# Optimization experiments

Measured on AMD Instinct MI355X. Metric: run time of the kernel, lower is better.

Reference implementation:

```python
import jax, jax.numpy as jnp
import numpy as np

F, V, D, B = 3, 512, 8192, 64


def setup_inputs() -> dict:
    key = jax.random.key(0)
    k1, k2 = jax.random.split(key)
    # bipolar (MAP) codebooks: (f, v, d) in {-1, +1}
    codebooks = jnp.sign(jax.random.normal(k1, (F, V, D), dtype=jnp.float32))
    codebooks = jnp.where(codebooks == 0, 1.0, codebooks)
    # ground-truth factors -> inputs = bind (elementwise product) of one codevector per factor
    idx = jax.random.randint(k2, (B, F), 0, V)
    picked = codebooks[jnp.arange(F)[None, :], idx]          # (b, f, d)
    inputs = jnp.prod(picked, axis=1)                         # (b, d)
    # init estimates: bundle (superposition) of each codebook, signed, broadcast to batch
    init = jnp.sign(jnp.sum(codebooks, axis=1))               # (f, d)
    init = jnp.where(init == 0, 1.0, init)
    init_estimates = jnp.broadcast_to(init, (B, F, D)).astype(jnp.float32)
    return {"inputs": inputs, "init_estimates": init_estimates,
            "codebooks": codebooks, "iterations": 10}


def reference(inputs, init_estimates, codebooks, iterations):
    f = init_estimates.shape[-2]

    def step(est):
        # MAP inverse is identity; inv_others[:, j] = prod_{i != j} est[:, i]
        rolled = jnp.stack([jnp.roll(est, i, axis=-2) for i in range(1, f)], axis=-2)  # (b,f,f-1,d)
        inv_others = jnp.prod(rolled, axis=-2)                 # (b, f, d)  multibind
        new_est = inputs[:, None, :] * inv_others              # bind       (b, f, d)
        sim = jnp.einsum('bfd,fvd->bfv', new_est, codebooks)   # codebook similarity
        return jnp.sign(jnp.einsum('bfv,fvd->bfd', sim, codebooks))

    def cond(c):
        est, old, cnt, done = c
        return (cnt < iterations) & jnp.logical_not(done)

    def body(c):
        est, old, cnt, done = c
        new = step(est)
        done = jnp.all(new == old)
        return (new, new, cnt + 1, done)

    carry0 = (init_estimates, init_estimates, jnp.int32(0), jnp.array(False))
    est, _, cnt, _ = jax.lax.while_loop(cond, body, carry0)

    # cleanup: nearest codevector per factor (argmax dot similarity)
    sims = jnp.einsum('bfd,fvd->bfv', est, codebooks)
    outcome = jnp.argmax(sims, axis=-1)                        # (b, f) int indices
    return outcome, cnt - 1
```

## Files before the change

kernel.cpp:

```cpp
#include <hip/hip_runtime.h>

#define F 3
#define V 512
#define D 8192
#define B 64
#define ITERS 10
#define DW 256

typedef __bf16 bf16_t;
typedef __bf16 bf16x8 __attribute__((ext_vector_type(8)));
typedef float f32x4 __attribute__((ext_vector_type(4)));
typedef unsigned int u32;
typedef unsigned short u16;
typedef u16 u16x8 __attribute__((ext_vector_type(8)));
typedef unsigned long long u64;


__global__ __launch_bounds__(256) void k_init_tr(const float* __restrict__ Csrc,
                                                 u32* __restrict__ Cbits,
                                                 u32* __restrict__ CbTb,
                                                 int* __restrict__ flags) {
  int f = blockIdx.z, vt = blockIdx.y, dt = blockIdx.x;
  __shared__ bf16_t tile[64 * 65];
  int t = threadIdx.x;
  int lane = t & 63;
  int v0 = vt * 64, d0 = dt * 64;
  if (f == 0 && vt == 0 && dt == 0 && t < 32) flags[t] = 0;
#pragma unroll
  for (int p = 0; p < 16; ++p) {
    int q = t + 256 * p;
    int i = q >> 6, j = q & 63;
    float x = Csrc[((long)(f * V + v0 + i)) * D + d0 + j];
    tile[i * 65 + j] = (bf16_t)x;
    u64 bal = __ballot(x < 0.f);
    if (lane == 0) {
      int v = v0 + i;
      uint2 wp;
      wp.x = (u32)(bal & 0xffffffffull);
      wp.y = (u32)(bal >> 32);
      *(uint2*)&Cbits[(((f * 64 + (dt >> 1)) * 512) + v) * 4 + (dt & 1) * 2] = wp;
    }
  }
  __syncthreads();
#pragma unroll
  for (int p = 0; p < 16; ++p) {
    int q = t + 256 * p;
    int jj = q >> 6, ii = q & 63;
    float xv = (float)tile[ii * 65 + jj];
    u64 bal = __ballot(xv < 0.f);
    if (lane == 0) {
      int d = d0 + jj;
      uint2 wp;
      wp.x = (u32)(bal & 0xffffffffull);
      wp.y = (u32)(bal >> 32);
      *(uint2*)&CbTb[((long)f * D + d) * 16 + vt * 2] = wp;
    }
  }
}

__global__ void k_init_pack(const float* __restrict__ inputs, const float* __restrict__ ie,
                            u32* __restrict__ in_bits, u32* __restrict__ es0,
                            u32* __restrict__ ez0, int* __restrict__ flags) {
  int tid = blockIdx.x * blockDim.x + threadIdx.x;
  int lane = tid & 63;
  int gw = tid >> 6;
  int NW = (gridDim.x * blockDim.x) >> 6;
  const int IN_W = B * (D / 64);
  const int EST_W = B * F * (D / 64);
  for (int c = gw; c < IN_W + EST_W; c += NW) {
    if (c < IN_W) {
      int b = c >> 7, dc = c & 127;
      float x = inputs[(long)b * D + dc * 64 + lane];
      u64 bal = __ballot(x < 0.f);
      if (lane == 0) {
        in_bits[b * DW + dc * 2] = (u32)(bal & 0xffffffffull);
        in_bits[b * DW + dc * 2 + 1] = (u32)(bal >> 32);
      }
    } else {
      int cc = c - IN_W;
      int bf = cc >> 7, dc = cc & 127;
      float x = ie[(long)bf * D + dc * 64 + lane];
      u64 bs = __ballot(x < 0.f);
      u64 bz = __ballot(x == 0.f);
      if (lane == 0) {
        es0[bf * DW + dc * 2] = (u32)(bs & 0xffffffffull);
        es0[bf * DW + dc * 2 + 1] = (u32)(bs >> 32);
        ez0[bf * DW + dc * 2] = (u32)(bz & 0xffffffffull);
        ez0[bf * DW + dc * 2 + 1] = (u32)(bz >> 32);
        if (bz) atomicOr(&flags[16], 1);
      }
    }
  }
}

__global__ __launch_bounds__(512) void k_sim(const u32* __restrict__ Cbits,
                                             const u32* __restrict__ in_bits,
                                             const u32* __restrict__ es0,
                                             const u32* __restrict__ ez0,
                                             const u32* __restrict__ es1,
                                             const u32* __restrict__ ez1,
                                             int* __restrict__ sim,
                                             const int* __restrict__ flags, int iter) {
  const int t = threadIdx.x, lane = t & 63, w = t >> 6;
  const int gw = blockIdx.x * 8 + w;
  const int vg = gw & 7, b = (gw >> 3) & 63, fs = gw >> 9;
  const bool is_final = (iter >= ITERS);
  const u32 *es, *ez;
  if (is_final) {
    int first0 = ITERS;
    for (int i = 0; i < ITERS; ++i)
      if (flags[i] == 0) { first0 = i; break; }
    int par = (first0 < ITERS) ? ((first0 + 1) & 1) : 0;
    es = par ? es1 : es0;
    ez = par ? ez1 : ez0;
  } else {
    for (int i = 0; i < iter; ++i)
      if (flags[i] == 0) return;
    es = (iter & 1) ? es1 : es0;
    ez = (iter & 1) ? ez1 : ez0;
  }
  const int hz = flags[16];

  u32 As[4], Az[4];
  if (is_final) {
    const int i0 = (b * F + fs) * DW;
#pragma unroll
    for (int r = 0; r < 4; ++r) As[r] = es[i0 + r * 64 + lane];
    if (hz) {
#pragma unroll
      for (int r = 0; r < 4; ++r) Az[r] = ~ez[i0 + r * 64 + lane];
    }
  } else {
    const int f1 = (fs + 1) % 3, f2 = (fs + 2) % 3;
    const int a0 = (b * F + f1) * DW, a1 = (b * F + f2) * DW;
    const int n0 = b * DW;
#pragma unroll
    for (int r = 0; r < 4; ++r) {
      int o = r * 64 + lane;
      As[r] = in_bits[n0 + o] ^ es[a0 + o] ^ es[a1 + o];
    }
    if (hz) {
#pragma unroll
      for (int r = 0; r < 4; ++r) {
        int o = r * 64 + lane;
        Az[r] = ~(ez[a0 + o] | ez[a1 + o]);
      }
    }
  }

  int nzc = D;
  if (hz) {
    int p0 = 0;
#pragma unroll
    for (int r = 0; r < 4; ++r) p0 += __popc(Az[r]);
    for (int off = 32; off; off >>= 1) p0 += __shfl_xor(p0, off, 64);
    nzc = p0;
  }

  int acc = 0;
  const uint4* Cp = (const uint4*)Cbits + ((long)fs * 64) * 512 + vg * 64 + lane;
  if (!hz) {
#pragma unroll
    for (int r = 0; r < 4; ++r) {
#pragma unroll
      for (int i = 0; i < 16; ++i) {
        uint4 c = Cp[(r * 16 + i) * 512];
        const int k = i * 4;
        u32 a;
        a = (u32)__builtin_amdgcn_readlane((int)As[r], k + 0); acc += __popc(c.x ^ a);
        a = (u32)__builtin_amdgcn_readlane((int)As[r], k + 1); acc += __popc(c.y ^ a);
        a = (u32)__builtin_amdgcn_readlane((int)As[r], k + 2); acc += __popc(c.z ^ a);
        a = (u32)__builtin_amdgcn_readlane((int)As[r], k + 3); acc += __popc(c.w ^ a);
      }
    }
  } else {
#pragma unroll
    for (int r = 0; r < 4; ++r) {
#pragma unroll
      for (int i = 0; i < 16; ++i) {
        uint4 c = Cp[(r * 16 + i) * 512];
        const int k = i * 4;
        u32 a, z;
        a = (u32)__builtin_amdgcn_readlane((int)As[r], k + 0);
        z = (u32)__builtin_amdgcn_readlane((int)Az[r], k + 0); acc += __popc((c.x ^ a) & z);
        a = (u32)__builtin_amdgcn_readlane((int)As[r], k + 1);
        z = (u32)__builtin_amdgcn_readlane((int)Az[r], k + 1); acc += __popc((c.y ^ a) & z);
        a = (u32)__builtin_amdgcn_readlane((int)As[r], k + 2);
        z = (u32)__builtin_amdgcn_readlane((int)Az[r], k + 2); acc += __popc((c.z ^ a) & z);
        a = (u32)__builtin_amdgcn_readlane((int)As[r], k + 3);
        z = (u32)__builtin_amdgcn_readlane((int)Az[r], k + 3); acc += __popc((c.w ^ a) & z);
      }
    }
  }
  sim[(fs * B + b) * V + vg * 64 + lane] = nzc - 2 * acc;
}

__global__ __launch_bounds__(512) void k_upd(const int* __restrict__ sim,
                                             const u32* __restrict__ CbTb,
                                             u32* __restrict__ es0, u32* __restrict__ ez0,
                                             u32* __restrict__ es1, u32* __restrict__ ez1,
                                             int* __restrict__ flags, int iter) {
  const int fu = blockIdx.x >> 6;
  const int dt = blockIdx.x & 63, d0 = dt * 128;
  for (int i = 0; i < iter; ++i)
    if (flags[i] == 0) return;
  const u32* esIn = (iter & 1) ? es1 : es0;
  const u32* ezIn = (iter & 1) ? ez1 : ez0;
  u32* esOut = (iter & 1) ? es0 : es1;
  u32* ezOut = (iter & 1) ? ez0 : ez1;
  const int* simf = sim + fu * (B * V);

  __shared__ __attribute__((aligned(16))) bf16_t lAh[64 * 88];
  __shared__ __attribute__((aligned(16))) bf16_t lAl[64 * 88];
  __shared__ __attribute__((aligned(16))) bf16_t lB[128 * 88];

  const int t = threadIdx.x;
  const int lane = t & 63, w = t >> 6;
  const int lm = lane & 15, quad = lane >> 4;
  const int wd = w & 3, wm = w >> 2;

  f32x4 zero = {0.f, 0.f, 0.f, 0.f};
  f32x4 accH[2][2], accL[2][2];
#pragma unroll
  for (int m = 0; m < 2; ++m)
#pragma unroll
    for (int nt = 0; nt < 2; ++nt) { accH[m][nt] = zero; accL[m][nt] = zero; }

  for (int c = 0; c < 8; ++c) {
    const int vb = c * 64;
    __syncthreads();
    {
      int b8 = t >> 3, vv = (t & 7) * 8;
      const int* sp = simf + b8 * V + vb + vv;
      int4 sa = ((const int4*)sp)[0];
      int4 sb = ((const int4*)sp)[1];
      int si[8] = {sa.x, sa.y, sa.z, sa.w, sb.x, sb.y, sb.z, sb.w};
#pragma unroll
      for (int i = 0; i < 8; ++i) {
        lAh[b8 * 88 + vv + i] = (bf16_t)(float)(si[i] >> 8);
        lAl[b8 * 88 + vv + i] = (bf16_t)(float)(si[i] & 255);
      }
    }
#pragma unroll
    for (int p = 0; p < 2; ++p) {
      int q = t + 512 * p;
      int r = q >> 3, vv = (q & 7) * 8;
      u32 bits = CbTb[((long)fu * D + d0 + r) * 16 + ((vb + vv) >> 5)];
      int sh = (vb + vv) & 31;
      u16x8 o;
#pragma unroll
      for (int i = 0; i < 8; ++i)
        o[i] = (u16)(0x3F80u | (((bits >> (sh + i)) & 1u) << 15));
      *(u16x8*)&lB[r * 88 + vv] = o;
    }
    __syncthreads();
#pragma unroll
    for (int ks2 = 0; ks2 < 2; ++ks2) {
      const int kb = ks2 * 32 + quad * 8;
      bf16x8 bf0 = *(const bf16x8*)&lB[(wd * 32 + lm) * 88 + kb];
      bf16x8 bf1 = *(const bf16x8*)&lB[(wd * 32 + 16 + lm) * 88 + kb];
#pragma unroll
      for (int m = 0; m < 2; ++m) {
        const int mt = wm * 2 + m;
        bf16x8 ah = *(const bf16x8*)&lAh[(mt * 16 + lm) * 88 + kb];
        bf16x8 al = *(const bf16x8*)&lAl[(mt * 16 + lm) * 88 + kb];
        accH[m][0] = __builtin_amdgcn_mfma_f32_16x16x32_bf16(ah, bf0, accH[m][0], 0, 0, 0);
        accH[m][1] = __builtin_amdgcn_mfma_f32_16x16x32_bf16(ah, bf1, accH[m][1], 0, 0, 0);
        accL[m][0] = __builtin_amdgcn_mfma_f32_16x16x32_bf16(al, bf0, accL[m][0], 0, 0, 0);
        accL[m][1] = __builtin_amdgcn_mfma_f32_16x16x32_bf16(al, bf1, accL[m][1], 0, 0, 0);
      }
    }
  }
  const int W = dt * 4 + wd;
  bool anyd = false, zf = false;
#pragma unroll
  for (int m = 0; m < 2; ++m)
#pragma unroll
    for (int r = 0; r < 4; ++r) {
      float v0 = 256.f * accH[m][0][r] + accL[m][0][r];
      float v1 = 256.f * accH[m][1][r] + accL[m][1][r];
      u64 s0 = __ballot(v0 < 0.f);
      u64 s1 = __ballot(v1 < 0.f);
      u64 z0 = __ballot(v0 == 0.f);
      u64 z1 = __ballot(v1 == 0.f);
      zf |= ((z0 | z1) != 0ull);
      if (lm == 0) {
        u32 ws = (u32)((s0 >> (quad * 16)) & 0xffffull) |
                 (((u32)((s1 >> (quad * 16)) & 0xffffull)) << 16);
        u32 wz = (u32)((z0 >> (quad * 16)) & 0xffffull) |
                 (((u32)((z1 >> (quad * 16)) & 0xffffull)) << 16);
        int b = (wm * 2 + m) * 16 + quad * 4 + r;
        int idx = (b * F + fu) * DW + W;
        anyd |= (esIn[idx] != ws) || (ezIn[idx] != wz);
        esOut[idx] = ws;
        ezOut[idx] = wz;
      }
    }
  if (__any(anyd) && lane == 0) atomicOr(&flags[iter], 1);
  if (zf && lane == 0) atomicOr(&flags[16], 1);
}

__global__ __launch_bounds__(64) void k_out(const int* __restrict__ sim,
                                            const int* __restrict__ flags,
                                            int* __restrict__ out) {
  int bid = blockIdx.x;
  int b = bid / F, f = bid % F;
  int lane = threadIdx.x;
  const int* row = sim + (f * B + b) * V;
  int best = -2147483647;
  int bidx = 0;
#pragma unroll
  for (int i = 0; i < V / 64; ++i) {
    int v = lane + 64 * i;
    int x = row[v];
    if (x > best) { best = x; bidx = v; }
  }
  for (int off = 32; off; off >>= 1) {
    int ov = __shfl_down(best, off, 64);
    int oi = __shfl_down(bidx, off, 64);
    if (ov > best || (ov == best && oi < bidx)) { best = ov; bidx = oi; }
  }
  if (lane == 0) out[b * F + f] = bidx;
  if (bid == 0 && lane == 0) {
    int first0 = ITERS;
    for (int i = 0; i < ITERS; ++i) {
      if (flags[i] == 0) { first0 = i; break; }
    }
    int cnt = (first0 < ITERS) ? (first0 + 1) : ITERS;
    out[B * F] = cnt - 1;
  }
}

extern "C" void kernel_launch(void* const* d_in, const int* in_sizes, int n_in,
                              void* d_out, int out_size, void* d_ws, size_t ws_size,
                              hipStream_t stream) {
  const float* inputs    = (const float*)d_in[0];
  const float* init_est  = (const float*)d_in[1];
  const float* codebooks = (const float*)d_in[2];

  char* w = (char*)d_ws;
  size_t o = 0;
  auto alloc = [&](size_t bytes) -> void* {
    void* p = w + o;
    o = (o + bytes + 255) & ~(size_t)255;
    return p;
  };
  u32* Cbits   = (u32*)alloc((size_t)F * 64 * 512 * 4 * 4);
  u32* CbTb    = (u32*)alloc((size_t)F * D * 16 * 4);
  u32* in_bits = (u32*)alloc((size_t)B * DW * 4);
  u32* es0     = (u32*)alloc((size_t)B * F * DW * 4);
  u32* ez0     = (u32*)alloc((size_t)B * F * DW * 4);
  u32* es1     = (u32*)alloc((size_t)B * F * DW * 4);
  u32* ez1     = (u32*)alloc((size_t)B * F * DW * 4);
  int* sim     = (int*)alloc((size_t)F * B * V * 4);
  int* flags   = (int*)alloc(128);

  k_init_tr<<<dim3(128, 8, 3), 256, 0, stream>>>(codebooks, Cbits, CbTb, flags);
  k_init_pack<<<1024, 256, 0, stream>>>(inputs, init_est, in_bits, es0, ez0, flags);

  for (int j = 0; j < ITERS; ++j) {
    k_sim<<<192, 512, 0, stream>>>(Cbits, in_bits, es0, ez0, es1, ez1, sim, flags, j);
    k_upd<<<192, 512, 0, stream>>>(sim, CbTb, es0, ez0, es1, ez1, flags, j);
  }
  k_sim<<<192, 512, 0, stream>>>(Cbits, in_bits, es0, ez0, es1, ez1, sim, flags, ITERS);
  k_out<<<B * F, 64, 0, stream>>>(sim, flags, (int*)d_out);
}
```

Measured before the change: 533.9 us.

## Fuse iteration loop into one persistent kernel with software grid barriers

Replaces the 21 per-iteration launches of k_sim/k_upd plus k_out with a single persistent kernel of 192 blocks that alternates similarity and update phases, separated by an atomic counter/generation grid barrier. Convergence is checked in-kernel so all blocks break out together, and the argmax output step runs in the same kernel. This removes launch gaps and the early-exit flag scanning, in exchange for relying on all 192 blocks being co-resident and on the correctness of the hand-written barrier's fences.

```diff
diff --git a/kernel.cpp b/kernel.cpp
--- a/kernel.cpp
+++ b/kernel.cpp
@@ -6,6 +6,7 @@
 #define B 64
 #define ITERS 10
 #define DW 256
+#define NBLK 192
 
 typedef __bf16 bf16_t;
 typedef __bf16 bf16x8 __attribute__((ext_vector_type(8)));
@@ -15,6 +16,10 @@
 typedef u16 u16x8 __attribute__((ext_vector_type(8)));
 typedef unsigned long long u64;
 
+
+__device__ inline int aload(const int* p) {
+  return __hip_atomic_load((int*)p, __ATOMIC_RELAXED, __HIP_MEMORY_SCOPE_AGENT);
+}
 
 __global__ __launch_bounds__(256) void k_init_tr(const float* __restrict__ Csrc,
                                                  u32* __restrict__ Cbits,
@@ -25,7 +30,7 @@
   int t = threadIdx.x;
   int lane = t & 63;
   int v0 = vt * 64, d0 = dt * 64;
-  if (f == 0 && vt == 0 && dt == 0 && t < 32) flags[t] = 0;
+  if (f == 0 && vt == 0 && dt == 0 && t < 64) flags[t] = 0;
 #pragma unroll
   for (int p = 0; p < 16; ++p) {
     int q = t + 256 * p;
@@ -93,240 +98,248 @@
   }
 }
 
-__global__ __launch_bounds__(512) void k_sim(const u32* __restrict__ Cbits,
-                                             const u32* __restrict__ in_bits,
-                                             const u32* __restrict__ es0,
-                                             const u32* __restrict__ ez0,
-                                             const u32* __restrict__ es1,
-                                             const u32* __restrict__ ez1,
-                                             int* __restrict__ sim,
-                                             const int* __restrict__ flags, int iter) {
-  const int t = threadIdx.x, lane = t & 63, w = t >> 6;
-  const int gw = blockIdx.x * 8 + w;
-  const int vg = gw & 7, b = (gw >> 3) & 63, fs = gw >> 9;
-  const bool is_final = (iter >= ITERS);
-  const u32 *es, *ez;
-  if (is_final) {
-    int first0 = ITERS;
-    for (int i = 0; i < ITERS; ++i)
-      if (flags[i] == 0) { first0 = i; break; }
-    int par = (first0 < ITERS) ? ((first0 + 1) & 1) : 0;
-    es = par ? es1 : es0;
-    ez = par ? ez1 : ez0;
-  } else {
-    for (int i = 0; i < iter; ++i)
-      if (flags[i] == 0) return;
-    es = (iter & 1) ? es1 : es0;
-    ez = (iter & 1) ? ez1 : ez0;
-  }
-  const int hz = flags[16];
-
-  u32 As[4], Az[4];
-  if (is_final) {
-    const int i0 = (b * F + fs) * DW;
-#pragma unroll
-    for (int r = 0; r < 4; ++r) As[r] = es[i0 + r * 64 + lane];
-    if (hz) {
-#pragma unroll
-      for (int r = 0; r < 4; ++r) Az[r] = ~ez[i0 + r * 64 + lane];
-    }
-  } else {
-    const int f1 = (fs + 1) % 3, f2 = (fs + 2) % 3;
-    const int a0 = (b * F + f1) * DW, a1 = (b * F + f2) * DW;
-    const int n0 = b * DW;
-#pragma unroll
-    for (int r = 0; r < 4; ++r) {
-      int o = r * 64 + lane;
-      As[r] = in_bits[n0 + o] ^ es[a0 + o] ^ es[a1 + o];
-    }
-    if (hz) {
-#pragma unroll
-      for (int r = 0; r < 4; ++r) {
-        int o = r * 64 + lane;
-        Az[r] = ~(ez[a0 + o] | ez[a1 + o]);
-      }
-    }
-  }
-
-  int nzc = D;
-  if (hz) {
-    int p0 = 0;
-#pragma unroll
-    for (int r = 0; r < 4; ++r) p0 += __popc(Az[r]);
-    for (int off = 32; off; off >>= 1) p0 += __shfl_xor(p0, off, 64);
-    nzc = p0;
-  }
-
-  int acc = 0;
-  const uint4* Cp = (const uint4*)Cbits + ((long)fs * 64) * 512 + vg * 64 + lane;
-  if (!hz) {
-#pragma unroll
-    for (int r = 0; r < 4; ++r) {
-#pragma unroll
-      for (int i = 0; i < 16; ++i) {
-        uint4 c = Cp[(r * 16 + i) * 512];
-        const int k = i * 4;
-        u32 a;
-        a = (u32)__builtin_amdgcn_readlane((int)As[r], k + 0); acc += __popc(c.x ^ a);
-        a = (u32)__builtin_amdgcn_readlane((int)As[r], k + 1); acc += __popc(c.y ^ a);
-        a = (u32)__builtin_amdgcn_readlane((int)As[r], k + 2); acc += __popc(c.z ^ a);
-        a = (u32)__builtin_amdgcn_readlane((int)As[r], k + 3); acc += __popc(c.w ^ a);
-      }
-    }
-  } else {
-#pragma unroll
-    for (int r = 0; r < 4; ++r) {
-#pragma unroll
-      for (int i = 0; i < 16; ++i) {
-        uint4 c = Cp[(r * 16 + i) * 512];
-        const int k = i * 4;
-        u32 a, z;
-        a = (u32)__builtin_amdgcn_readlane((int)As[r], k + 0);
-        z = (u32)__builtin_amdgcn_readlane((int)Az[r], k + 0); acc += __popc((c.x ^ a) & z);
-        a = (u32)__builtin_amdgcn_readlane((int)As[r], k + 1);
-        z = (u32)__builtin_amdgcn_readlane((int)Az[r], k + 1); acc += __popc((c.y ^ a) & z);
-        a = (u32)__builtin_amdgcn_readlane((int)As[r], k + 2);
-        z = (u32)__builtin_amdgcn_readlane((int)Az[r], k + 2); acc += __popc((c.z ^ a) & z);
-        a = (u32)__builtin_amdgcn_readlane((int)As[r], k + 3);
-        z = (u32)__builtin_amdgcn_readlane((int)Az[r], k + 3); acc += __popc((c.w ^ a) & z);
-      }
-    }
-  }
-  sim[(fs * B + b) * V + vg * 64 + lane] = nzc - 2 * acc;
-}
-
-__global__ __launch_bounds__(512) void k_upd(const int* __restrict__ sim,
-                                             const u32* __restrict__ CbTb,
-                                             u32* __restrict__ es0, u32* __restrict__ ez0,
-                                             u32* __restrict__ es1, u32* __restrict__ ez1,
-                                             int* __restrict__ flags, int iter) {
-  const int fu = blockIdx.x >> 6;
-  const int dt = blockIdx.x & 63, d0 = dt * 128;
-  for (int i = 0; i < iter; ++i)
-    if (flags[i] == 0) return;
-  const u32* esIn = (iter & 1) ? es1 : es0;
-  const u32* ezIn = (iter & 1) ? ez1 : ez0;
-  u32* esOut = (iter & 1) ? es0 : es1;
-  u32* ezOut = (iter & 1) ? ez0 : ez1;
-  const int* simf = sim + fu * (B * V);
-
+__device__ inline void grid_sync(int* counter, int* gen) {
+  __syncthreads();
+  if (threadIdx.x == 0) {
+    __builtin_amdgcn_fence(__ATOMIC_RELEASE, "agent");
+    int g = __hip_atomic_load(gen, __ATOMIC_RELAXED, __HIP_MEMORY_SCOPE_AGENT);
+    int a = __hip_atomic_fetch_add(counter, 1, __ATOMIC_RELAXED, __HIP_MEMORY_SCOPE_AGENT);
+    if (a == NBLK - 1) {
+      __hip_atomic_store(counter, 0, __ATOMIC_RELAXED, __HIP_MEMORY_SCOPE_AGENT);
+      __hip_atomic_store(gen, g + 1, __ATOMIC_RELAXED, __HIP_MEMORY_SCOPE_AGENT);
+    } else {
+      while (__hip_atomic_load(gen, __ATOMIC_RELAXED, __HIP_MEMORY_SCOPE_AGENT) == g)
+        __builtin_amdgcn_s_sleep(4);
+    }
+    __builtin_amdgcn_fence(__ATOMIC_ACQUIRE, "agent");
+  }
+  __syncthreads();
+}
+
+__global__ __launch_bounds__(512) void k_fused(
+    const u32* __restrict__ Cbits, const u32* __restrict__ in_bits,
+    u32* __restrict__ es0, u32* __restrict__ ez0,
+    u32* __restrict__ es1, u32* __restrict__ ez1,
+    const u32* __restrict__ CbTb, int* __restrict__ sim,
+    int* __restrict__ flags, int* __restrict__ out) {
   __shared__ __attribute__((aligned(16))) bf16_t lAh[64 * 88];
   __shared__ __attribute__((aligned(16))) bf16_t lAl[64 * 88];
   __shared__ __attribute__((aligned(16))) bf16_t lB[128 * 88];
 
-  const int t = threadIdx.x;
-  const int lane = t & 63, w = t >> 6;
+  int* bar_cnt = flags + 32;
+  int* bar_gen = flags + 40;
+
+  const int bid = blockIdx.x;
+  const int t = threadIdx.x, lane = t & 63, w = t >> 6;
   const int lm = lane & 15, quad = lane >> 4;
+  const int gwv = bid * 8 + w;
+  const int vg = gwv & 7, bb = (gwv >> 3) & 63, fs = gwv >> 9;
+  const int fu = bid >> 6, dt = bid & 63, d0 = dt * 128;
   const int wd = w & 3, wm = w >> 2;
 
-  f32x4 zero = {0.f, 0.f, 0.f, 0.f};
-  f32x4 accH[2][2], accL[2][2];
-#pragma unroll
-  for (int m = 0; m < 2; ++m)
-#pragma unroll
-    for (int nt = 0; nt < 2; ++nt) { accH[m][nt] = zero; accL[m][nt] = zero; }
-
-  for (int c = 0; c < 8; ++c) {
-    const int vb = c * 64;
-    __syncthreads();
-    {
-      int b8 = t >> 3, vv = (t & 7) * 8;
-      const int* sp = simf + b8 * V + vb + vv;
-      int4 sa = ((const int4*)sp)[0];
-      int4 sb = ((const int4*)sp)[1];
-      int si[8] = {sa.x, sa.y, sa.z, sa.w, sb.x, sb.y, sb.z, sb.w};
-#pragma unroll
-      for (int i = 0; i < 8; ++i) {
-        lAh[b8 * 88 + vv + i] = (bf16_t)(float)(si[i] >> 8);
-        lAl[b8 * 88 + vv + i] = (bf16_t)(float)(si[i] & 255);
-      }
-    }
-#pragma unroll
-    for (int p = 0; p < 2; ++p) {
-      int q = t + 512 * p;
-      int r = q >> 3, vv = (q & 7) * 8;
-      u32 bits = CbTb[((long)fu * D + d0 + r) * 16 + ((vb + vv) >> 5)];
-      int sh = (vb + vv) & 31;
-      u16x8 o;
-#pragma unroll
-      for (int i = 0; i < 8; ++i)
-        o[i] = (u16)(0x3F80u | (((bits >> (sh + i)) & 1u) << 15));
-      *(u16x8*)&lB[r * 88 + vv] = o;
-    }
-    __syncthreads();
-#pragma unroll
-    for (int ks2 = 0; ks2 < 2; ++ks2) {
-      const int kb = ks2 * 32 + quad * 8;
-      bf16x8 bf0 = *(const bf16x8*)&lB[(wd * 32 + lm) * 88 + kb];
-      bf16x8 bf1 = *(const bf16x8*)&lB[(wd * 32 + 16 + lm) * 88 + kb];
-#pragma unroll
-      for (int m = 0; m < 2; ++m) {
-        const int mt = wm * 2 + m;
-        bf16x8 ah = *(const bf16x8*)&lAh[(mt * 16 + lm) * 88 + kb];
-        bf16x8 al = *(const bf16x8*)&lAl[(mt * 16 + lm) * 88 + kb];
-        accH[m][0] = __builtin_amdgcn_mfma_f32_16x16x32_bf16(ah, bf0, accH[m][0], 0, 0, 0);
-        accH[m][1] = __builtin_amdgcn_mfma_f32_16x16x32_bf16(ah, bf1, accH[m][1], 0, 0, 0);
-        accL[m][0] = __builtin_amdgcn_mfma_f32_16x16x32_bf16(al, bf0, accL[m][0], 0, 0, 0);
-        accL[m][1] = __builtin_amdgcn_mfma_f32_16x16x32_bf16(al, bf1, accL[m][1], 0, 0, 0);
-      }
-    }
-  }
-  const int W = dt * 4 + wd;
-  bool anyd = false, zf = false;
-#pragma unroll
-  for (int m = 0; m < 2; ++m)
-#pragma unroll
-    for (int r = 0; r < 4; ++r) {
-      float v0 = 256.f * accH[m][0][r] + accL[m][0][r];
-      float v1 = 256.f * accH[m][1][r] + accL[m][1][r];
-      u64 s0 = __ballot(v0 < 0.f);
-      u64 s1 = __ballot(v1 < 0.f);
-      u64 z0 = __ballot(v0 == 0.f);
-      u64 z1 = __ballot(v1 == 0.f);
-      zf |= ((z0 | z1) != 0ull);
-      if (lm == 0) {
-        u32 ws = (u32)((s0 >> (quad * 16)) & 0xffffull) |
-                 (((u32)((s1 >> (quad * 16)) & 0xffffull)) << 16);
-        u32 wz = (u32)((z0 >> (quad * 16)) & 0xffffull) |
-                 (((u32)((z1 >> (quad * 16)) & 0xffffull)) << 16);
-        int b = (wm * 2 + m) * 16 + quad * 4 + r;
-        int idx = (b * F + fu) * DW + W;
-        anyd |= (esIn[idx] != ws) || (ezIn[idx] != wz);
-        esOut[idx] = ws;
-        ezOut[idx] = wz;
-      }
-    }
-  if (__any(anyd) && lane == 0) atomicOr(&flags[iter], 1);
-  if (zf && lane == 0) atomicOr(&flags[16], 1);
-}
-
-__global__ __launch_bounds__(64) void k_out(const int* __restrict__ sim,
-                                            const int* __restrict__ flags,
-                                            int* __restrict__ out) {
-  int bid = blockIdx.x;
-  int b = bid / F, f = bid % F;
-  int lane = threadIdx.x;
-  const int* row = sim + (f * B + b) * V;
-  int best = -2147483647;
-  int bidx = 0;
-#pragma unroll
-  for (int i = 0; i < V / 64; ++i) {
-    int v = lane + 64 * i;
-    int x = row[v];
-    if (x > best) { best = x; bidx = v; }
-  }
-  for (int off = 32; off; off >>= 1) {
-    int ov = __shfl_down(best, off, 64);
-    int oi = __shfl_down(bidx, off, 64);
-    if (ov > best || (ov == best && oi < bidx)) { best = ov; bidx = oi; }
-  }
-  if (lane == 0) out[b * F + f] = bidx;
-  if (bid == 0 && lane == 0) {
-    int first0 = ITERS;
-    for (int i = 0; i < ITERS; ++i) {
-      if (flags[i] == 0) { first0 = i; break; }
-    }
-    int cnt = (first0 < ITERS) ? (first0 + 1) : ITERS;
+  int parity = 0;
+  int done_iter = ITERS;
+  int hz = aload(&flags[16]);
+
+  auto sim_phase = [&](bool is_final) {
+    const u32* es = parity ? es1 : es0;
+    const u32* ez = parity ? ez1 : ez0;
+    u32 As[4], Az[4];
+    if (is_final) {
+      const int i0 = (bb * F + fs) * DW;
+#pragma unroll
+      for (int r = 0; r < 4; ++r) As[r] = es[i0 + r * 64 + lane];
+      if (hz) {
+#pragma unroll
+        for (int r = 0; r < 4; ++r) Az[r] = ~ez[i0 + r * 64 + lane];
+      }
+    } else {
+      const int f1 = (fs + 1) % 3, f2 = (fs + 2) % 3;
+      const int a0 = (bb * F + f1) * DW, a1 = (bb * F + f2) * DW;
+      const int n0 = bb * DW;
+#pragma unroll
+      for (int r = 0; r < 4; ++r) {
+        int o = r * 64 + lane;
+        As[r] = in_bits[n0 + o] ^ es[a0 + o] ^ es[a1 + o];
+      }
+      if (hz) {
+#pragma unroll
+        for (int r = 0; r < 4; ++r) {
+          int o = r * 64 + lane;
+          Az[r] = ~(ez[a0 + o] | ez[a1 + o]);
+        }
+      }
+    }
+
+    int nzc = D;
+    if (hz) {
+      int p0 = 0;
+#pragma unroll
+      for (int r = 0; r < 4; ++r) p0 += __popc(Az[r]);
+      for (int off = 32; off; off >>= 1) p0 += __shfl_xor(p0, off, 64);
+      nzc = p0;
+    }
+
+    int acc = 0;
+    const uint4* Cp = (const uint4*)Cbits + ((long)fs * 64) * 512 + vg * 64 + lane;
+    if (!hz) {
+#pragma unroll
+      for (int r = 0; r < 4; ++r) {
+#pragma unroll
+        for (int i = 0; i < 16; ++i) {
+          uint4 c = Cp[(r * 16 + i) * 512];
+          const int k = i * 4;
+          u32 a;
+          a = (u32)__builtin_amdgcn_readlane((int)As[r], k + 0); acc += __popc(c.x ^ a);
+          a = (u32)__builtin_amdgcn_readlane((int)As[r], k + 1); acc += __popc(c.y ^ a);
+          a = (u32)__builtin_amdgcn_readlane((int)As[r], k + 2); acc += __popc(c.z ^ a);
+          a = (u32)__builtin_amdgcn_readlane((int)As[r], k + 3); acc += __popc(c.w ^ a);
+        }
+      }
+    } else {
+#pragma unroll
+      for (int r = 0; r < 4; ++r) {
+#pragma unroll
+        for (int i = 0; i < 16; ++i) {
+          uint4 c = Cp[(r * 16 + i) * 512];
+          const int k = i * 4;
+          u32 a, z;
+          a = (u32)__builtin_amdgcn_readlane((int)As[r], k + 0);
+          z = (u32)__builtin_amdgcn_readlane((int)Az[r], k + 0); acc += __popc((c.x ^ a) & z);
+          a = (u32)__builtin_amdgcn_readlane((int)As[r], k + 1);
+          z = (u32)__builtin_amdgcn_readlane((int)Az[r], k + 1); acc += __popc((c.y ^ a) & z);
+          a = (u32)__builtin_amdgcn_readlane((int)As[r], k + 2);
+          z = (u32)__builtin_amdgcn_readlane((int)Az[r], k + 2); acc += __popc((c.z ^ a) & z);
+          a = (u32)__builtin_amdgcn_readlane((int)As[r], k + 3);
+          z = (u32)__builtin_amdgcn_readlane((int)Az[r], k + 3); acc += __popc((c.w ^ a) & z);
+        }
+      }
+    }
+    sim[(fs * B + bb) * V + vg * 64 + lane] = nzc - 2 * acc;
+  };
+
+  auto upd_phase = [&](int j) {
+    const u32* esIn = parity ? es1 : es0;
+    const u32* ezIn = parity ? ez1 : ez0;
+    u32* esOut = parity ? es0 : es1;
+    u32* ezOut = parity ? ez0 : ez1;
+    const int* simf = sim + fu * (B * V);
+
+    f32x4 zero = {0.f, 0.f, 0.f, 0.f};
+    f32x4 accH[2][2], accL[2][2];
+#pragma unroll
+    for (int m = 0; m < 2; ++m)
+#pragma unroll
+      for (int nt = 0; nt < 2; ++nt) { accH[m][nt] = zero; accL[m][nt] = zero; }
+
+    for (int c = 0; c < 8; ++c) {
+      const int vb = c * 64;
+      __syncthreads();
+      {
+        int b8 = t >> 3, vv = (t & 7) * 8;
+        const int* sp = simf + b8 * V + vb + vv;
+        int4 sa = ((const int4*)sp)[0];
+        int4 sb = ((const int4*)sp)[1];
+        int si[8] = {sa.x, sa.y, sa.z, sa.w, sb.x, sb.y, sb.z, sb.w};
+#pragma unroll
+        for (int i = 0; i < 8; ++i) {
+          lAh[b8 * 88 + vv + i] = (bf16_t)(float)(si[i] >> 8);
+          lAl[b8 * 88 + vv + i] = (bf16_t)(float)(si[i] & 255);
+        }
+      }
+#pragma unroll
+      for (int p = 0; p < 2; ++p) {
+        int q = t + 512 * p;
+        int r = q >> 3, vv = (q & 7) * 8;
+        u32 bits = CbTb[((long)fu * D + d0 + r) * 16 + ((vb + vv) >> 5)];
+        int sh = (vb + vv) & 31;
+        u16x8 o;
+#pragma unroll
+        for (int i = 0; i < 8; ++i)
+          o[i] = (u16)(0x3F80u | (((bits >> (sh + i)) & 1u) << 15));
+        *(u16x8*)&lB[r * 88 + vv] = o;
+      }
+      __syncthreads();
+#pragma unroll
+      for (int ks2 = 0; ks2 < 2; ++ks2) {
+        const int kb = ks2 * 32 + quad * 8;
+        bf16x8 bf0 = *(const bf16x8*)&lB[(wd * 32 + lm) * 88 + kb];
+        bf16x8 bf1 = *(const bf16x8*)&lB[(wd * 32 + 16 + lm) * 88 + kb];
+#pragma unroll
+        for (int m = 0; m < 2; ++m) {
+          const int mt = wm * 2 + m;
+          bf16x8 ah = *(const bf16x8*)&lAh[(mt * 16 + lm) * 88 + kb];
+          bf16x8 al = *(const bf16x8*)&lAl[(mt * 16 + lm) * 88 + kb];
+          accH[m][0] = __builtin_amdgcn_mfma_f32_16x16x32_bf16(ah, bf0, accH[m][0], 0, 0, 0);
+          accH[m][1] = __builtin_amdgcn_mfma_f32_16x16x32_bf16(ah, bf1, accH[m][1], 0, 0, 0);
+          accL[m][0] = __builtin_amdgcn_mfma_f32_16x16x32_bf16(al, bf0, accL[m][0], 0, 0, 0);
+          accL[m][1] = __builtin_amdgcn_mfma_f32_16x16x32_bf16(al, bf1, accL[m][1], 0, 0, 0);
+        }
+      }
+    }
+    const int W = dt * 4 + wd;
+    bool anyd = false, zf = false;
+#pragma unroll
+    for (int m = 0; m < 2; ++m)
+#pragma unroll
+      for (int r = 0; r < 4; ++r) {
+        float v0 = 256.f * accH[m][0][r] + accL[m][0][r];
+        float v1 = 256.f * accH[m][1][r] + accL[m][1][r];
+        u64 s0 = __ballot(v0 < 0.f);
+        u64 s1 = __ballot(v1 < 0.f);
+        u64 z0 = __ballot(v0 == 0.f);
+        u64 z1 = __ballot(v1 == 0.f);
+        zf |= ((z0 | z1) != 0ull);
+        if (lm == 0) {
+          u32 ws = (u32)((s0 >> (quad * 16)) & 0xffffull) |
+                   (((u32)((s1 >> (quad * 16)) & 0xffffull)) << 16);
+          u32 wz = (u32)((z0 >> (quad * 16)) & 0xffffull) |
+                   (((u32)((z1 >> (quad * 16)) & 0xffffull)) << 16);
+          int b = (wm * 2 + m) * 16 + quad * 4 + r;
+          int idx = (b * F + fu) * DW + W;
+          anyd |= (esIn[idx] != ws) || (ezIn[idx] != wz);
+          esOut[idx] = ws;
+          ezOut[idx] = wz;
+        }
+      }
+    if (__any(anyd) && lane == 0) atomicOr(&flags[j], 1);
+    if (zf && lane == 0) atomicOr(&flags[16], 1);
+  };
+
+  for (int j = 0; j < ITERS; ++j) {
+    sim_phase(false);
+    grid_sync(bar_cnt, bar_gen);
+    upd_phase(j);
+    grid_sync(bar_cnt, bar_gen);
+    int conv = aload(&flags[j]);
+    hz = aload(&flags[16]);
+    parity ^= 1;
+    if (conv == 0) { done_iter = j; break; }
+  }
+
+  sim_phase(true);
+  grid_sync(bar_cnt, bar_gen);
+
+  if (t < 64) {
+    int b = bid / F, f = bid % F;
+    const int* row = sim + (f * B + b) * V;
+    int best = -2147483647;
+    int bidx = 0;
+#pragma unroll
+    for (int i = 0; i < V / 64; ++i) {
+      int v = lane + 64 * i;
+      int x = row[v];
+      if (x > best) { best = x; bidx = v; }
+    }
+    for (int off = 32; off; off >>= 1) {
+      int ov = __shfl_down(best, off, 64);
+      int oi = __shfl_down(bidx, off, 64);
+      if (ov > best || (ov == best && oi < bidx)) { best = ov; bidx = oi; }
+    }
+    if (lane == 0) out[b * F + f] = bidx;
+  }
+  if (bid == 0 && t == 0) {
+    int cnt = (done_iter < ITERS) ? (done_iter + 1) : ITERS;
     out[B * F] = cnt - 1;
   }
 }
@@ -353,15 +366,10 @@
   u32* es1     = (u32*)alloc((size_t)B * F * DW * 4);
   u32* ez1     = (u32*)alloc((size_t)B * F * DW * 4);
   int* sim     = (int*)alloc((size_t)F * B * V * 4);
-  int* flags   = (int*)alloc(128);
+  int* flags   = (int*)alloc(256);
 
   k_init_tr<<<dim3(128, 8, 3), 256, 0, stream>>>(codebooks, Cbits, CbTb, flags);
   k_init_pack<<<1024, 256, 0, stream>>>(inputs, init_est, in_bits, es0, ez0, flags);
-
-  for (int j = 0; j < ITERS; ++j) {
-    k_sim<<<192, 512, 0, stream>>>(Cbits, in_bits, es0, ez0, es1, ez1, sim, flags, j);
-    k_upd<<<192, 512, 0, stream>>>(sim, CbTb, es0, ez0, es1, ez1, flags, j);
-  }
-  k_sim<<<192, 512, 0, stream>>>(Cbits, in_bits, es0, ez0, es1, ez1, sim, flags, ITERS);
-  k_out<<<B * F, 64, 0, stream>>>(sim, flags, (int*)d_out);
-}
+  k_fused<<<NBLK, 512, 0, stream>>>(Cbits, in_bits, es0, ez0, es1, ez1, CbTb, sim,
+                                    flags, (int*)d_out);
+}
```

After: 685.4 us. +28.4%, slower.
